# Performance work log

Measured on AMD Instinct MI355X. Metric: run time of the kernel, lower is better.

Reference implementation:

```python
import jax, jax.numpy as jnp
import numpy as np
import math

B, N, D, H = 2, 64, 256, 8
DK = D // H


def setup_inputs() -> dict:
    key = jax.random.key(0)
    ks = jax.random.split(key, 12)
    s = 1.0 / math.sqrt(D)
    inp = {
        "state": jax.random.normal(ks[0], (B, N, N, D), dtype=jnp.float32),
        "mask": jnp.zeros((B, N, N, N), dtype=bool),
        "W_lk": jax.random.normal(ks[1], (D, D), dtype=jnp.float32) * s,
        "b_lk": jnp.zeros((D,), dtype=jnp.float32),
        "W_rk": jax.random.normal(ks[2], (D, D), dtype=jnp.float32) * s,
        "b_rk": jnp.zeros((D,), dtype=jnp.float32),
        "W_lv": jax.random.normal(ks[3], (D, D), dtype=jnp.float32) * s,
        "b_lv": jnp.zeros((D,), dtype=jnp.float32),
        "W_rv": jax.random.normal(ks[4], (D, D), dtype=jnp.float32) * s,
        "b_rv": jnp.zeros((D,), dtype=jnp.float32),
        "W_o": jax.random.normal(ks[5], (D, D), dtype=jnp.float32) * s,
        "b_o": jnp.zeros((D,), dtype=jnp.float32),
    }
    return inp


def _proj(x, W, b):
    # torch nn.Linear: x @ W.T + b, then view to heads
    y = jnp.einsum('bxyd,ed->bxye', x, W) + b
    return y.reshape(B, N, N, H, DK)


def reference(state, mask, W_lk, b_lk, W_rk, b_rk, W_lv, b_lv, W_rv, b_rv, W_o, b_o):
    left_k = _proj(state, W_lk, b_lk)   # [B,N,N,H,DK]
    right_k = _proj(state, W_rk, b_rk)
    left_v = _proj(state, W_lv, b_lv)
    right_v = _proj(state, W_rv, b_rv)

    # triangle-style scores over node triples (x, a, y): [B,N,N,N,H]
    scores = jnp.einsum('bxahd,bayhd->bxayh', left_k, right_k) / math.sqrt(DK)
    scores = jnp.where(mask[..., None], jnp.float32(-1000.0), scores)
    att = jax.nn.softmax(scores, axis=2)  # softmax over intermediate node a

    # val[b,x,a,y,h,d] = left_v[b,x,a,h,d] * right_v[b,a,y,h,d] (materialized as in torch)
    val = jnp.einsum('bxahd,bayhd->bxayhd', left_v, right_v)
    x = jnp.einsum('bxayh,bxayhd->bxyhd', att, val)  # sum over a
    x = x.reshape(B, N, N, D)
    return jnp.einsum('bxyd,ed->bxye', x, W_o) + b_o
```

## Files before the change

### kernel.cpp

```cpp
#include <hip/hip_runtime.h>

#define B 2
#define N 64
#define D 256
#define H 8
#define DK 32
#define M (B * N * N)

typedef __attribute__((ext_vector_type(8))) short bf16x8;
typedef __attribute__((ext_vector_type(4))) float f32x4;

#define OFF_LK 0
#define OFF_RK 256
#define OFF_LV 512
#define OFF_RV 768

__device__ __forceinline__ ushort f2b(float f) {
    union { float f; unsigned u; } v; v.f = f;
    unsigned r = v.u + 0x7fffu + ((v.u >> 16) & 1u);
    return (ushort)(r >> 16);
}
__device__ __forceinline__ float b2f(ushort u) {
    union { unsigned u; float f; } v; v.u = ((unsigned)u) << 16; return v.f;
}
__device__ __forceinline__ void cvt8(float4 raw, float* f) {
    const ushort* s = (const ushort*)&raw;
#pragma unroll
    for (int j = 0; j < 8; ++j) f[j] = b2f(s[j]);
}

__global__ __launch_bounds__(256) void cast_all(const float* __restrict__ state,
                                                const float* __restrict__ W_lk, const float* __restrict__ W_rk,
                                                const float* __restrict__ W_lv, const float* __restrict__ W_rv,
                                                const float* __restrict__ W_o,
                                                const float* __restrict__ b_lk, const float* __restrict__ b_rk,
                                                const float* __restrict__ b_lv, const float* __restrict__ b_rv,
                                                const float* __restrict__ b_o,
                                                ushort* __restrict__ state_bf,
                                                ushort* __restrict__ Wcat,
                                                float* __restrict__ bias_cat) {
    const int gid = blockIdx.x * 256 + threadIdx.x;
    const float* Ws[5] = {W_lk, W_rk, W_lv, W_rv, W_o};
    const float* bs[5] = {b_lk, b_rk, b_lv, b_rv, b_o};

    if (gid < 1280) bias_cat[gid] = bs[gid >> 8][gid & 255];

    if (gid < 524288) {
        float4 v = *(const float4*)&state[(size_t)gid * 4];
        ushort4 o = {f2b(v.x), f2b(v.y), f2b(v.z), f2b(v.w)};
        *(ushort4*)&state_bf[(size_t)gid * 4] = o;
    } else {
        int u = gid - 524288;
        int row = u >> 6;
        int k4 = (u & 63) * 4;
        const float* W = Ws[row >> 8];
        float4 v = *(const float4*)&W[(size_t)(row & 255) * 256 + k4];
        ushort4 o = {f2b(v.x), f2b(v.y), f2b(v.z), f2b(v.w)};
        *(ushort4*)&Wcat[(size_t)row * 256 + k4] = o;
    }
}

#define LDK 56

template <int BF16OUT>
__global__ __launch_bounds__(256) void gemm_mfma(const ushort* __restrict__ A,
                                                 const ushort* __restrict__ Bw,
                                                 const float* __restrict__ bias,
                                                 void* __restrict__ Cv, int ldc) {
    __shared__ __align__(16) ushort As[128 * LDK];
    __shared__ __align__(16) ushort Bs[128 * LDK];
    const int tid = threadIdx.x;
    const int lane = tid & 63;
    const int wave = tid >> 6;
    const int wm = (wave & 1) * 64;
    const int wn = (wave >> 1) * 64;
    const int row0 = blockIdx.x * 128;
    const int col0 = blockIdx.y * 128;

    const int srow = tid >> 2;
    const int skq = (tid & 3) * 8;

    const int fr = lane & 15;
    const int fk = (lane >> 4) * 8;

    f32x4 acc[4][4] = {};

    for (int k0 = 0; k0 < 256; k0 += 32) {
        float4 av0 = *(const float4*)&A[(size_t)(row0 + srow) * 256 + k0 + skq];
        float4 av1 = *(const float4*)&A[(size_t)(row0 + 64 + srow) * 256 + k0 + skq];
        float4 bv0 = *(const float4*)&Bw[(size_t)(col0 + srow) * 256 + k0 + skq];
        float4 bv1 = *(const float4*)&Bw[(size_t)(col0 + 64 + srow) * 256 + k0 + skq];
        __syncthreads();
        *(float4*)&As[srow * LDK + skq] = av0;
        *(float4*)&As[(64 + srow) * LDK + skq] = av1;
        *(float4*)&Bs[srow * LDK + skq] = bv0;
        *(float4*)&Bs[(64 + srow) * LDK + skq] = bv1;
        __syncthreads();

        bf16x8 af[4], bf[4];
#pragma unroll
        for (int i = 0; i < 4; ++i)
            af[i] = *(const bf16x8*)&As[(wm + i * 16 + fr) * LDK + fk];
#pragma unroll
        for (int j = 0; j < 4; ++j)
            bf[j] = *(const bf16x8*)&Bs[(wn + j * 16 + fr) * LDK + fk];
#pragma unroll
        for (int i = 0; i < 4; ++i)
#pragma unroll
            for (int j = 0; j < 4; ++j)
                acc[i][j] = __builtin_amdgcn_mfma_f32_16x16x32_bf16(af[i], bf[j], acc[i][j], 0, 0, 0);
    }

#pragma unroll
    for (int j = 0; j < 4; ++j) {
        const int col = col0 + wn + j * 16 + (lane & 15);
        const float bv = bias[col];
#pragma unroll
        for (int i = 0; i < 4; ++i) {
            const int rbase = row0 + wm + i * 16 + (lane >> 4) * 4;
#pragma unroll
            for (int r = 0; r < 4; ++r) {
                float o = acc[i][j][r] + bv;
                if (BF16OUT) ((ushort*)Cv)[(size_t)(rbase + r) * ldc + col] = f2b(o);
                else ((float*)Cv)[(size_t)(rbase + r) * ldc + col] = o;
            }
        }
    }
}

__global__ __launch_bounds__(256) void scores_kernel(const ushort* __restrict__ P,
                                                     const unsigned char* __restrict__ mask,
                                                     ushort* __restrict__ att) {
    const int a = blockIdx.x, h = blockIdx.y, b = blockIdx.z;
    __shared__ __align__(16) float LKs[DK][68];
    __shared__ __align__(16) float RKs[DK][68];
    const int tid = threadIdx.x;

    {
        const int x = tid >> 2;
        const int d0 = (tid & 3) * 8;
        float f[8];
        float4 v = *(const float4*)&P[(((size_t)b * N + x) * N + a) * 1024 + OFF_LK + h * DK + d0];
        cvt8(v, f);
#pragma unroll
        for (int j = 0; j < 8; ++j) LKs[d0 + j][x] = f[j];
        float4 w = *(const float4*)&P[(((size_t)b * N + a) * N + x) * 1024 + OFF_RK + h * DK + d0];
        cvt8(w, f);
#pragma unroll
        for (int j = 0; j < 8; ++j) RKs[d0 + j][x] = f[j];
    }
    __syncthreads();

    const int tx = tid & 15, ty = tid >> 4;
    float acc[4][4] = {};
#pragma unroll
    for (int d = 0; d < DK; ++d) {
        float4 xa = *(const float4*)&LKs[d][ty * 4];
        float4 yb = *(const float4*)&RKs[d][tx * 4];
        acc[0][0] += xa.x * yb.x; acc[0][1] += xa.x * yb.y; acc[0][2] += xa.x * yb.z; acc[0][3] += xa.x * yb.w;
        acc[1][0] += xa.y * yb.x; acc[1][1] += xa.y * yb.y; acc[1][2] += xa.y * yb.z; acc[1][3] += xa.y * yb.w;
        acc[2][0] += xa.z * yb.x; acc[2][1] += xa.z * yb.y; acc[2][2] += xa.z * yb.z; acc[2][3] += xa.z * yb.w;
        acc[3][0] += xa.w * yb.x; acc[3][1] += xa.w * yb.y; acc[3][2] += xa.w * yb.z; acc[3][3] += xa.w * yb.w;
    }

    const float scale = 0.17677669529663687f;
    ushort* tile = &att[(((size_t)(b * H + h) * N + a) * N) * N];
#pragma unroll
    for (int i = 0; i < 4; ++i) {
        const int x = ty * 4 + i;
        uchar4 mk = *(const uchar4*)&mask[(((size_t)b * N + x) * N + a) * N + tx * 4];
        ushort4 o;
        o.x = f2b(mk.x ? -1000.0f : acc[i][0] * scale);
        o.y = f2b(mk.y ? -1000.0f : acc[i][1] * scale);
        o.z = f2b(mk.z ? -1000.0f : acc[i][2] * scale);
        o.w = f2b(mk.w ? -1000.0f : acc[i][3] * scale);
        *(ushort4*)&tile[x * 64 + tx * 4] = o;
    }
}

__global__ __launch_bounds__(256) void softmax_a(ushort* __restrict__ att) {
    const int bh = blockIdx.x >> 4;
    const int chunk = blockIdx.x & 15;
    ushort* base = att + (size_t)bh * (N * N * N) + chunk * 256 + threadIdx.x;

    float v[64];
    float m = -1e30f;
#pragma unroll
    for (int a = 0; a < 64; ++a) {
        v[a] = b2f(base[(size_t)a * (N * N)]);
        m = fmaxf(m, v[a]);
    }
    float s = 0.0f;
#pragma unroll
    for (int a = 0; a < 64; ++a) {
        v[a] = __expf(v[a] - m);
        s += v[a];
    }
    const float inv = 1.0f / s;
#pragma unroll
    for (int a = 0; a < 64; ++a) {
        base[(size_t)a * (N * N)] = f2b(v[a] * inv);
    }
}

__global__ __launch_bounds__(256) void combine_kernel(const ushort* __restrict__ P,
                                                      const ushort* __restrict__ att,
                                                      ushort* __restrict__ xbuf) {
    __shared__ __align__(16) float2 LVs2[8 * 16 * 16];
    __shared__ __align__(16) float2 RVs2[8 * 16 * 18];
    __shared__ __align__(16) float atts[16 * 164];

    const int bh = blockIdx.z;
    const int b = bh >> 3, h = bh & 7;
    const int x0 = blockIdx.x * 16, y0 = blockIdx.y * 16;
    const int tid = threadIdx.x;
    const int x_l = tid >> 4, dp = tid & 15;

    float2 acc[16] = {};

    for (int ac = 0; ac < N; ac += 8) {
        __syncthreads();
        {
            const int r = tid >> 1, q = tid & 1;
            float f[16];
            {
                int x = r >> 3, a = r & 7;
                const ushort* src = &P[(((size_t)b * N + x0 + x) * N + ac + a) * 1024 + OFF_LV + h * DK + q * 16];
                cvt8(*(const float4*)&src[0], f);
                cvt8(*(const float4*)&src[8], f + 8);
                float2* dst = &LVs2[(a * 16 + x) * 16 + q * 8];
#pragma unroll
                for (int j = 0; j < 4; ++j)
                    *(float4*)&dst[2 * j] = make_float4(f[4 * j], f[4 * j + 1], f[4 * j + 2], f[4 * j + 3]);
            }
            {
                int a = r >> 4, y = r & 15;
                const ushort* src = &P[(((size_t)b * N + ac + a) * N + y0 + y) * 1024 + OFF_RV + h * DK + q * 16];
                cvt8(*(const float4*)&src[0], f);
                cvt8(*(const float4*)&src[8], f + 8);
#pragma unroll
                for (int m2 = 0; m2 < 8; ++m2)
                    RVs2[(a * 16 + q * 8 + m2) * 18 + y] = make_float2(f[2 * m2], f[2 * m2 + 1]);
            }
            {
                int x = r >> 3, a = r & 7;
                const ushort* src = &att[(((size_t)bh * N + ac + a) * N + x0 + x) * N + y0 + q * 8];
                cvt8(*(const float4*)&src[0], f);
                float* dst = &atts[x * 164 + a * 20 + q * 8];
                *(float4*)&dst[0] = make_float4(f[0], f[1], f[2], f[3]);
                *(float4*)&dst[4] = make_float4(f[4], f[5], f[6], f[7]);
            }
        }
        __syncthreads();

#pragma unroll
        for (int a = 0; a < 8; ++a) {
            float2 lv = LVs2[(a * 16 + x_l) * 16 + dp];
            const float* wrow = &atts[x_l * 164 + a * 20];
            const float2* rvrow = &RVs2[(a * 16 + dp) * 18];
            float4 wq[4];
#pragma unroll
            for (int j = 0; j < 4; ++j) wq[j] = *(const float4*)&wrow[j * 4];
            const float* wv = (const float*)wq;
#pragma unroll
            for (int yq = 0; yq < 8; ++yq) {
                float4 rv4 = *(const float4*)&rvrow[yq * 2];
                float w0 = wv[yq * 2], w1 = wv[yq * 2 + 1];
                acc[yq * 2].x += (w0 * lv.x) * rv4.x;
                acc[yq * 2].y += (w0 * lv.y) * rv4.y;
                acc[yq * 2 + 1].x += (w1 * lv.x) * rv4.z;
                acc[yq * 2 + 1].y += (w1 * lv.y) * rv4.w;
            }
        }
    }

#pragma unroll
    for (int y = 0; y < 16; ++y) {
        ushort2 o = {f2b(acc[y].x), f2b(acc[y].y)};
        *(ushort2*)&xbuf[(((size_t)b * N + x0 + x_l) * N + y0 + y) * D + h * DK + 2 * dp] = o;
    }
}

extern "C" void kernel_launch(void* const* d_in, const int* in_sizes, int n_in,
                              void* d_out, int out_size, void* d_ws, size_t ws_size,
                              hipStream_t stream) {
    const float* state = (const float*)d_in[0];
    const unsigned char* mask = (const unsigned char*)d_in[1];
    const float* W_lk = (const float*)d_in[2];
    const float* b_lk = (const float*)d_in[3];
    const float* W_rk = (const float*)d_in[4];
    const float* b_rk = (const float*)d_in[5];
    const float* W_lv = (const float*)d_in[6];
    const float* b_lv = (const float*)d_in[7];
    const float* W_rv = (const float*)d_in[8];
    const float* b_rv = (const float*)d_in[9];
    const float* W_o = (const float*)d_in[10];
    const float* b_o = (const float*)d_in[11];
    float* out = (float*)d_out;

    char* ws = (char*)d_ws;
    ushort* P_bf = (ushort*)ws;
    ws += (size_t)M * 1024 * 2;
    ushort* att_bf = (ushort*)ws;
    ws += (size_t)B * H * N * N * N * 2;
    float* bias_cat = (float*)ws;
    ws += 1280 * 4;
    ushort* state_bf = (ushort*)ws;
    ws += (size_t)M * D * 2;
    ushort* Wcat = (ushort*)ws;
    ws += (size_t)1280 * 256 * 2;
    ushort* xbuf_bf = (ushort*)ws;

    cast_all<<<2368, 256, 0, stream>>>(state, W_lk, W_rk, W_lv, W_rv, W_o,
                                       b_lk, b_rk, b_lv, b_rv, b_o,
                                       state_bf, Wcat, bias_cat);
    gemm_mfma<1><<<dim3(M / 128, 8), 256, 0, stream>>>(state_bf, Wcat, bias_cat, P_bf, 1024);
    scores_kernel<<<dim3(N, H, B), 256, 0, stream>>>(P_bf, mask, att_bf);
    softmax_a<<<B * H * 16, 256, 0, stream>>>(att_bf);
    combine_kernel<<<dim3(4, 4, B * H), 256, 0, stream>>>(P_bf, att_bf, xbuf_bf);
    gemm_mfma<0><<<dim3(M / 128, 2), 256, 0, stream>>>(xbuf_bf, Wcat + 1024 * 256, bias_cat + 1024, out, 256);
}
```

Measured before the change: 149.6 us.

## Fuse online softmax into combine kernel and use direct global-to-LDS loads in GEMM

```diff
diff --git a/kernel.cpp b/kernel.cpp
--- a/kernel.cpp
+++ b/kernel.cpp
@@ -27,6 +27,12 @@
     const ushort* s = (const ushort*)&raw;
 #pragma unroll
     for (int j = 0; j < 8; ++j) f[j] = b2f(s[j]);
+}
+
+__device__ __forceinline__ void glds16(const ushort* g, ushort* l) {
+    __builtin_amdgcn_global_load_lds(
+        (const __attribute__((address_space(1))) unsigned int*)g,
+        (__attribute__((address_space(3))) unsigned int*)l, 16, 0, 0);
 }
 
 __global__ __launch_bounds__(256) void cast_all(const float* __restrict__ state,
@@ -60,15 +66,13 @@
     }
 }
 
-#define LDK 56
-
 template <int BF16OUT>
 __global__ __launch_bounds__(256) void gemm_mfma(const ushort* __restrict__ A,
                                                  const ushort* __restrict__ Bw,
                                                  const float* __restrict__ bias,
                                                  void* __restrict__ Cv, int ldc) {
-    __shared__ __align__(16) ushort As[128 * LDK];
-    __shared__ __align__(16) ushort Bs[128 * LDK];
+    __shared__ __align__(16) ushort As[128 * 32];
+    __shared__ __align__(16) ushort Bs[128 * 32];
     const int tid = threadIdx.x;
     const int lane = tid & 63;
     const int wave = tid >> 6;
@@ -77,8 +81,17 @@
     const int row0 = blockIdx.x * 128;
     const int col0 = blockIdx.y * 128;
 
-    const int srow = tid >> 2;
-    const int skq = (tid & 3) * 8;
+    const int lr = lane >> 2;
+    const int lkq = (lane & 3) * 8;
+
+    const ushort* gA0 = A + (size_t)(row0 + wave * 32 + lr) * 256 + lkq;
+    const ushort* gA1 = gA0 + 16 * 256;
+    const ushort* gB0 = Bw + (size_t)(col0 + wave * 32 + lr) * 256 + lkq;
+    const ushort* gB1 = gB0 + 16 * 256;
+    ushort* lA0 = &As[(wave * 32) * 32];
+    ushort* lA1 = &As[(wave * 32 + 16) * 32];
+    ushort* lB0 = &Bs[(wave * 32) * 32];
+    ushort* lB1 = &Bs[(wave * 32 + 16) * 32];
 
     const int fr = lane & 15;
     const int fk = (lane >> 4) * 8;
@@ -86,24 +99,20 @@
     f32x4 acc[4][4] = {};
 
     for (int k0 = 0; k0 < 256; k0 += 32) {
-        float4 av0 = *(const float4*)&A[(size_t)(row0 + srow) * 256 + k0 + skq];
-        float4 av1 = *(const float4*)&A[(size_t)(row0 + 64 + srow) * 256 + k0 + skq];
-        float4 bv0 = *(const float4*)&Bw[(size_t)(col0 + srow) * 256 + k0 + skq];
-        float4 bv1 = *(const float4*)&Bw[(size_t)(col0 + 64 + srow) * 256 + k0 + skq];
-        __syncthreads();
-        *(float4*)&As[srow * LDK + skq] = av0;
-        *(float4*)&As[(64 + srow) * LDK + skq] = av1;
-        *(float4*)&Bs[srow * LDK + skq] = bv0;
-        *(float4*)&Bs[(64 + srow) * LDK + skq] = bv1;
+        __syncthreads();
+        glds16(gA0 + k0, lA0);
+        glds16(gA1 + k0, lA1);
+        glds16(gB0 + k0, lB0);
+        glds16(gB1 + k0, lB1);
         __syncthreads();
 
         bf16x8 af[4], bf[4];
 #pragma unroll
         for (int i = 0; i < 4; ++i)
-            af[i] = *(const bf16x8*)&As[(wm + i * 16 + fr) * LDK + fk];
+            af[i] = *(const bf16x8*)&As[(wm + i * 16 + fr) * 32 + fk];
 #pragma unroll
         for (int j = 0; j < 4; ++j)
-            bf[j] = *(const bf16x8*)&Bs[(wn + j * 16 + fr) * LDK + fk];
+            bf[j] = *(const bf16x8*)&Bs[(wn + j * 16 + fr) * 32 + fk];
 #pragma unroll
         for (int i = 0; i < 4; ++i)
 #pragma unroll
@@ -178,43 +187,24 @@
     }
 }
 
-__global__ __launch_bounds__(256) void softmax_a(ushort* __restrict__ att) {
-    const int bh = blockIdx.x >> 4;
-    const int chunk = blockIdx.x & 15;
-    ushort* base = att + (size_t)bh * (N * N * N) + chunk * 256 + threadIdx.x;
-
-    float v[64];
-    float m = -1e30f;
-#pragma unroll
-    for (int a = 0; a < 64; ++a) {
-        v[a] = b2f(base[(size_t)a * (N * N)]);
-        m = fmaxf(m, v[a]);
-    }
-    float s = 0.0f;
-#pragma unroll
-    for (int a = 0; a < 64; ++a) {
-        v[a] = __expf(v[a] - m);
-        s += v[a];
-    }
-    const float inv = 1.0f / s;
-#pragma unroll
-    for (int a = 0; a < 64; ++a) {
-        base[(size_t)a * (N * N)] = f2b(v[a] * inv);
-    }
-}
-
 __global__ __launch_bounds__(256) void combine_kernel(const ushort* __restrict__ P,
                                                       const ushort* __restrict__ att,
                                                       ushort* __restrict__ xbuf) {
     __shared__ __align__(16) float2 LVs2[8 * 16 * 16];
     __shared__ __align__(16) float2 RVs2[8 * 16 * 18];
     __shared__ __align__(16) float atts[16 * 164];
+    __shared__ float mstate[16][17];
+    __shared__ float lstate[16][17];
+    __shared__ float alphas[16][17];
 
     const int bh = blockIdx.z;
     const int b = bh >> 3, h = bh & 7;
     const int x0 = blockIdx.x * 16, y0 = blockIdx.y * 16;
     const int tid = threadIdx.x;
     const int x_l = tid >> 4, dp = tid & 15;
+
+    mstate[x_l][dp] = -3.0e38f;
+    lstate[x_l][dp] = 0.0f;
 
     float2 acc[16] = {};
 
@@ -253,6 +243,36 @@
         }
         __syncthreads();
 
+        {
+            const int sx = x_l, sy = dp;
+            float s8[8];
+#pragma unroll
+            for (int a = 0; a < 8; ++a) s8[a] = atts[sx * 164 + a * 20 + sy];
+            float mc = s8[0];
+#pragma unroll
+            for (int a = 1; a < 8; ++a) mc = fmaxf(mc, s8[a]);
+            const float mold = mstate[sx][sy];
+            const float mnew = fmaxf(mold, mc);
+            const float alpha = __expf(mold - mnew);
+            float ps = 0.0f;
+#pragma unroll
+            for (int a = 0; a < 8; ++a) {
+                float p = __expf(s8[a] - mnew);
+                atts[sx * 164 + a * 20 + sy] = p;
+                ps += p;
+            }
+            lstate[sx][sy] = lstate[sx][sy] * alpha + ps;
+            mstate[sx][sy] = mnew;
+            alphas[sx][sy] = alpha;
+        }
+        __syncthreads();
+
+#pragma unroll
+        for (int y = 0; y < 16; ++y) {
+            float al = alphas[x_l][y];
+            acc[y].x *= al; acc[y].y *= al;
+        }
+
 #pragma unroll
         for (int a = 0; a < 8; ++a) {
             float2 lv = LVs2[(a * 16 + x_l) * 16 + dp];
@@ -276,7 +296,8 @@
 
 #pragma unroll
     for (int y = 0; y < 16; ++y) {
-        ushort2 o = {f2b(acc[y].x), f2b(acc[y].y)};
+        const float invl = 1.0f / lstate[x_l][y];
+        ushort2 o = {f2b(acc[y].x * invl), f2b(acc[y].y * invl)};
         *(ushort2*)&xbuf[(((size_t)b * N + x0 + x_l) * N + y0 + y) * D + h * DK + 2 * dp] = o;
     }
 }
@@ -316,7 +337,6 @@
                                        state_bf, Wcat, bias_cat);
     gemm_mfma<1><<<dim3(M / 128, 8), 256, 0, stream>>>(state_bf, Wcat, bias_cat, P_bf, 1024);
     scores_kernel<<<dim3(N, H, B), 256, 0, stream>>>(P_bf, mask, att_bf);
-    softmax_a<<<B * H * 16, 256, 0, stream>>>(att_bf);
     combine_kernel<<<dim3(4, 4, B * H), 256, 0, stream>>>(P_bf, att_bf, xbuf_bf);
     gemm_mfma<0><<<dim3(M / 128, 2), 256, 0, stream>>>(xbuf_bf, Wcat + 1024 * 256, bias_cat + 1024, out, 256);
 }
```

Measured after the change: 140.0 us. 6.4% less time.
